# Optimization experiments

Hardware: AMD Instinct MI355X
Metric: run time of the kernel (lower is better)

The kernel has to match this reference:

```python
import jax, jax.numpy as jnp
import numpy as np

B, IN, N, E = 2048, 1024, 64, 128
NEG_SLOPE = 0.01  # torch LeakyReLU default

def setup_inputs() -> dict:
    key = jax.random.key(0)
    k = jax.random.split(key, 5)
    scale_in = 1.0 / np.sqrt(IN)
    scale_ctx = 1.0 / np.sqrt(2 * E)
    return {
        "x": jax.random.normal(k[0], (B, IN), dtype=jnp.float32),
        # stacked per-concept Linear(in_features, 2*emb_size)
        "W_ctx": jax.random.uniform(k[1], (N, IN, 2 * E), jnp.float32, -scale_in, scale_in),
        "b_ctx": jax.random.uniform(k[2], (N, 2 * E), jnp.float32, -scale_in, scale_in),
        # shared Linear(2*emb_size, 1)
        "w_prob": jax.random.uniform(k[3], (2 * E,), jnp.float32, -scale_ctx, scale_ctx),
        "b_prob": jax.random.uniform(k[4], (), jnp.float32, -scale_ctx, scale_ctx),
    }

def reference(x, W_ctx, b_ctx, w_prob, b_prob):
    # context: [B, N, 2E] = LeakyReLU(x @ W_i + b_i) for all concepts i at once
    ctx = jnp.einsum("bi,nio->bno", x, W_ctx) + b_ctx
    ctx = jnp.where(ctx >= 0, ctx, NEG_SLOPE * ctx)
    # shared gate: [B, N]
    c_pred = jax.nn.sigmoid(jnp.einsum("bno,o->bn", ctx, w_prob) + b_prob)
    # gated blend of positive/negative halves -> [B, N, E]
    p = c_pred[..., None]
    c_emb = ctx[..., :E] * p + ctx[..., E:] * (1.0 - p)
    return c_emb, c_pred
```

## Files before the change

kernel.cpp:

```cpp
#include <hip/hip_runtime.h>
#include <hip/hip_bf16.h>

typedef __attribute__((ext_vector_type(4))) short short4v;
typedef __attribute__((ext_vector_type(8))) short short8v;
typedef __attribute__((ext_vector_type(4))) float floatx4;

#define B_ROWS 2048
#define K_DIM  1024
#define N_CON  64
#define TWO_E  256
#define E_DIM  128
#define BM     128
#define BK     64
#define A_STRIDE 72
#define B_STRIDE 72
#define LDSA_BYTES (BM * A_STRIDE * 2)
#define LDSB_BYTES (TWO_E * B_STRIDE * 2)
#define SMEM_BYTES (LDSA_BYTES + LDSB_BYTES)
#define EMB_ELEMS 16777216ULL

static __device__ inline unsigned short bf16bits(float f) {
    __hip_bfloat16 h = __float2bfloat16(f);
    unsigned short u;
    __builtin_memcpy(&u, &h, 2);
    return u;
}

__global__ void __launch_bounds__(256) transpose_w(const float* __restrict__ W,
                                                   unsigned short* __restrict__ Wt) {
    __shared__ unsigned int lds2[64 * 36];
    const int tid = threadIdx.x;
    const int ot = blockIdx.x, ktile = blockIdx.y, n = blockIdx.z;
    const float* src = W + ((size_t)n * K_DIM + (size_t)ktile * 64) * TWO_E + ot * 64;
    unsigned short* dst = Wt + ((size_t)n * TWO_E + (size_t)ot * 64) * K_DIM + ktile * 64;

    const int kp = tid >> 4;
    const int c  = (tid & 15) * 4;
#pragma unroll
    for (int it = 0; it < 2; ++it) {
        const int k0 = it * 32 + kp * 2;
        floatx4 r0 = *(const floatx4*)&src[(size_t)k0 * TWO_E + c];
        floatx4 r1 = *(const floatx4*)&src[(size_t)(k0 + 1) * TWO_E + c];
#pragma unroll
        for (int j = 0; j < 4; ++j) {
            unsigned int d = (unsigned int)bf16bits(r0[j]) |
                             ((unsigned int)bf16bits(r1[j]) << 16);
            lds2[(c + j) * 36 + it * 16 + kp] = d;
        }
    }
    __syncthreads();
#pragma unroll
    for (int it = 0; it < 2; ++it) {
        int q = it * 256 + tid;
        int o = q >> 3, kc = q & 7;
        short8v v = *(short8v*)&lds2[o * 36 + kc * 4];
        *(short8v*)&dst[(size_t)o * K_DIM + kc * 8] = v;
    }
}

template <bool PRET>
__global__ void __launch_bounds__(512, 4)
concept_kernel(const float* __restrict__ x,
               const float* __restrict__ Wc,
               const unsigned short* __restrict__ Wt,
               const float* __restrict__ bc,
               const float* __restrict__ wp,
               const float* __restrict__ bp,
               float* __restrict__ out) {
    __shared__ __align__(16) char smem[SMEM_BYTES];
    unsigned short* ldsA = (unsigned short*)smem;
    unsigned short* ldsB = (unsigned short*)(smem + LDSA_BYTES);

    const int tid  = threadIdx.x;
    const int wave = tid >> 6;
    const int lane = tid & 63;
    const int lg   = lane >> 4;
    const int l15  = lane & 15;
    const int h    = wave >> 2;
    const int og   = wave & 3;
    const int rb = blockIdx.x;
    const int n  = blockIdx.y;

    int otile[4];
#pragma unroll
    for (int oi = 0; oi < 4; ++oi) otile[oi] = og * 32 + (oi & 1) * 16 + (oi & 2) * 64;

    const float* xg = x + (size_t)rb * BM * K_DIM;

    floatx4 acc[4][4];
#pragma unroll
    for (int mi = 0; mi < 4; ++mi)
#pragma unroll
        for (int oi = 0; oi < 4; ++oi) acc[mi][oi] = (floatx4){0.f, 0.f, 0.f, 0.f};

    for (int kt = 0; kt < K_DIM; kt += BK) {
#pragma unroll
        for (int it = 0; it < 4; ++it) {
            int q = it * 512 + tid;
            int r = q >> 4, c = (q & 15) * 4;
            floatx4 v = *(const floatx4*)&xg[(size_t)r * K_DIM + kt + c];
            short4v b;
            b[0] = (short)bf16bits(v[0]);
            b[1] = (short)bf16bits(v[1]);
            b[2] = (short)bf16bits(v[2]);
            b[3] = (short)bf16bits(v[3]);
            *(short4v*)&ldsA[r * A_STRIDE + c] = b;
        }
        if (PRET) {
            const unsigned short* wtg = Wt + (size_t)n * TWO_E * K_DIM;
#pragma unroll
            for (int it = 0; it < 4; ++it) {
                int q = it * 512 + tid;
                int o = q >> 3, ck = q & 7;
                short8v v = *(const short8v*)&wtg[(size_t)o * K_DIM + kt + ck * 8];
                *(short8v*)&ldsB[o * B_STRIDE + ck * 8] = v;
            }
        } else {
            if (tid < 256) {
                const float* wg = Wc + (size_t)n * K_DIM * TWO_E;
#pragma unroll
                for (int it = 0; it < 8; ++it) {
                    short8v v;
#pragma unroll
                    for (int j = 0; j < 8; ++j)
                        v[j] = (short)bf16bits(wg[(size_t)(kt + it * 8 + j) * TWO_E + tid]);
                    *(short8v*)&ldsB[tid * B_STRIDE + it * 8] = v;
                }
            }
        }
        __syncthreads();

#pragma unroll
        for (int ks = 0; ks < 2; ++ks) {
            const int kof = ks * 32 + lg * 8;
            short8v af[4], bfr[4];
#pragma unroll
            for (int mi = 0; mi < 4; ++mi)
                af[mi] = *(short8v*)&ldsA[(h * 64 + mi * 16 + l15) * A_STRIDE + kof];
#pragma unroll
            for (int oi = 0; oi < 4; ++oi)
                bfr[oi] = *(short8v*)&ldsB[(otile[oi] + l15) * B_STRIDE + kof];
#pragma unroll
            for (int mi = 0; mi < 4; ++mi)
#pragma unroll
                for (int oi = 0; oi < 4; ++oi)
                    acc[mi][oi] = __builtin_amdgcn_mfma_f32_16x16x32_bf16(
                        af[mi], bfr[oi], acc[mi][oi], 0, 0, 0);
        }
        __syncthreads();
    }

    float biasf[4], wpf[4];
#pragma unroll
    for (int oi = 0; oi < 4; ++oi) {
        int o = otile[oi] + l15;
        biasf[oi] = bc[n * TWO_E + o];
        wpf[oi]  = wp[o];
    }
#pragma unroll
    for (int mi = 0; mi < 4; ++mi)
#pragma unroll
        for (int oi = 0; oi < 4; ++oi)
#pragma unroll
            for (int j = 0; j < 4; ++j) {
                float v = acc[mi][oi][j] + biasf[oi];
                acc[mi][oi][j] = v >= 0.f ? v : 0.01f * v;
            }

    float* partial = (float*)smem;
    float* pv      = (float*)(smem + 2048);

#pragma unroll
    for (int mi = 0; mi < 4; ++mi)
#pragma unroll
        for (int j = 0; j < 4; ++j) {
            float ps = 0.f;
#pragma unroll
            for (int oi = 0; oi < 4; ++oi) ps += acc[mi][oi][j] * wpf[oi];
            ps += __shfl_xor(ps, 1);
            ps += __shfl_xor(ps, 2);
            ps += __shfl_xor(ps, 4);
            ps += __shfl_xor(ps, 8);
            if (l15 == 0) partial[(h * 64 + mi * 16 + lg * 4 + j) * 4 + og] = ps;
        }
    __syncthreads();

    if (tid < 128) {
        float s = partial[tid * 4] + partial[tid * 4 + 1] + partial[tid * 4 + 2] +
                  partial[tid * 4 + 3] + bp[0];
        float p = 1.f / (1.f + __expf(-s));
        pv[tid] = p;
        size_t bi = (size_t)rb * BM + tid;
        out[EMB_ELEMS + bi * N_CON + n] = p;
    }
    __syncthreads();

#pragma unroll
    for (int mi = 0; mi < 4; ++mi)
#pragma unroll
        for (int oi = 0; oi < 2; ++oi)
#pragma unroll
            for (int j = 0; j < 4; ++j) {
                int row = h * 64 + mi * 16 + lg * 4 + j;
                int e = og * 32 + oi * 16 + l15;
                float p = pv[row];
                float v = acc[mi][oi][j] * p + acc[mi][oi + 2][j] * (1.f - p);
                size_t bi = (size_t)rb * BM + row;
                out[(bi * N_CON + n) * E_DIM + e] = v;
            }
}

extern "C" void kernel_launch(void* const* d_in, const int* in_sizes, int n_in,
                              void* d_out, int out_size, void* d_ws, size_t ws_size,
                              hipStream_t stream) {
    const float* x  = (const float*)d_in[0];
    const float* Wc = (const float*)d_in[1];
    const float* bc = (const float*)d_in[2];
    const float* wp = (const float*)d_in[3];
    const float* bp = (const float*)d_in[4];
    float* out = (float*)d_out;

    const size_t wt_bytes = (size_t)N_CON * K_DIM * TWO_E * 2;
    if (ws_size >= wt_bytes) {
        unsigned short* Wt = (unsigned short*)d_ws;
        transpose_w<<<dim3(4, 16, 64), 256, 0, stream>>>(Wc, Wt);
        concept_kernel<true><<<dim3(16, 64), 512, 0, stream>>>(x, Wc, Wt, bc, wp, bp, out);
    } else {
        concept_kernel<false><<<dim3(16, 64), 512, 0, stream>>>(x, Wc, nullptr, bc, wp, bp, out);
    }
}
```

Measured before the change: 205.3 us.

## Pre-convert x to bf16 and stream tiles into LDS via direct global-to-LDS loads

The prep kernel now also converts x to bf16 in the workspace, alongside the W transpose. The main kernel then loads both A and B tiles with global_load_lds 16-byte direct-to-LDS transfers instead of going through registers. The padded LDS strides are replaced by an XOR swizzle so bank conflicts stay low without padding. This removes the repeated per-block fp32 x reads and conversions and the VGPR staging, at the cost of an extra workspace buffer and a dependence on the swizzle matching the MFMA read pattern.

```diff
diff --git a/kernel.cpp b/kernel.cpp
--- a/kernel.cpp
+++ b/kernel.cpp
@@ -12,12 +12,12 @@
 #define E_DIM  128
 #define BM     128
 #define BK     64
-#define A_STRIDE 72
-#define B_STRIDE 72
-#define LDSA_BYTES (BM * A_STRIDE * 2)
-#define LDSB_BYTES (TWO_E * B_STRIDE * 2)
+#define LDSA_BYTES (BM * BK * 2)
+#define LDSB_BYTES (TWO_E * BK * 2)
 #define SMEM_BYTES (LDSA_BYTES + LDSB_BYTES)
 #define EMB_ELEMS 16777216ULL
+#define WT_BYTES  33554432ULL
+#define XB_BYTES  4194304ULL
 
 static __device__ inline unsigned short bf16bits(float f) {
     __hip_bfloat16 h = __float2bfloat16(f);
@@ -26,8 +26,17 @@
     return u;
 }
 
-__global__ void __launch_bounds__(256) transpose_w(const float* __restrict__ W,
-                                                   unsigned short* __restrict__ Wt) {
+static __device__ inline void dma16(const void* g, void* l) {
+    __builtin_amdgcn_global_load_lds(
+        (const __attribute__((address_space(1))) unsigned int*)g,
+        (__attribute__((address_space(3))) unsigned int*)l,
+        16, 0, 0);
+}
+
+__global__ void __launch_bounds__(256) prep(const float* __restrict__ W,
+                                            const float* __restrict__ x,
+                                            unsigned short* __restrict__ Wt,
+                                            unsigned short* __restrict__ xb) {
     __shared__ unsigned int lds2[64 * 36];
     const int tid = threadIdx.x;
     const int ot = blockIdx.x, ktile = blockIdx.y, n = blockIdx.z;
@@ -56,11 +65,18 @@
         short8v v = *(short8v*)&lds2[o * 36 + kc * 4];
         *(short8v*)&dst[(size_t)o * K_DIM + kc * 8] = v;
     }
+
+    const int bid = blockIdx.x + blockIdx.y * 4 + blockIdx.z * 64;
+    const size_t base = (size_t)bid * 512 + (size_t)tid * 2;
+    unsigned int d = (unsigned int)bf16bits(x[base]) |
+                     ((unsigned int)bf16bits(x[base + 1]) << 16);
+    ((unsigned int*)xb)[base >> 1] = d;
 }
 
 template <bool PRET>
 __global__ void __launch_bounds__(512, 4)
 concept_kernel(const float* __restrict__ x,
+               const unsigned short* __restrict__ xb,
                const float* __restrict__ Wc,
                const unsigned short* __restrict__ Wt,
                const float* __restrict__ bc,
@@ -68,8 +84,8 @@
                const float* __restrict__ bp,
                float* __restrict__ out) {
     __shared__ __align__(16) char smem[SMEM_BYTES];
-    unsigned short* ldsA = (unsigned short*)smem;
-    unsigned short* ldsB = (unsigned short*)(smem + LDSA_BYTES);
+    char* ldsA = smem;
+    char* ldsB = smem + LDSA_BYTES;
 
     const int tid  = threadIdx.x;
     const int wave = tid >> 6;
@@ -85,61 +101,73 @@
 #pragma unroll
     for (int oi = 0; oi < 4; ++oi) otile[oi] = og * 32 + (oi & 1) * 16 + (oi & 2) * 64;
 
+    floatx4 acc[4][4];
+#pragma unroll
+    for (int mi = 0; mi < 4; ++mi)
+#pragma unroll
+        for (int oi = 0; oi < 4; ++oi) acc[mi][oi] = (floatx4){0.f, 0.f, 0.f, 0.f};
+
+    const unsigned short* xrow  = PRET ? xb + (size_t)rb * BM * K_DIM : nullptr;
+    const unsigned short* wbase = PRET ? Wt + (size_t)n * TWO_E * K_DIM : nullptr;
     const float* xg = x + (size_t)rb * BM * K_DIM;
-
-    floatx4 acc[4][4];
-#pragma unroll
-    for (int mi = 0; mi < 4; ++mi)
-#pragma unroll
-        for (int oi = 0; oi < 4; ++oi) acc[mi][oi] = (floatx4){0.f, 0.f, 0.f, 0.f};
+    const float* wg = Wc + (size_t)n * K_DIM * TWO_E;
 
     for (int kt = 0; kt < K_DIM; kt += BK) {
-#pragma unroll
-        for (int it = 0; it < 4; ++it) {
-            int q = it * 512 + tid;
-            int r = q >> 4, c = (q & 15) * 4;
-            floatx4 v = *(const floatx4*)&xg[(size_t)r * K_DIM + kt + c];
-            short4v b;
-            b[0] = (short)bf16bits(v[0]);
-            b[1] = (short)bf16bits(v[1]);
-            b[2] = (short)bf16bits(v[2]);
-            b[3] = (short)bf16bits(v[3]);
-            *(short4v*)&ldsA[r * A_STRIDE + c] = b;
-        }
         if (PRET) {
-            const unsigned short* wtg = Wt + (size_t)n * TWO_E * K_DIM;
+#pragma unroll
+            for (int it = 0; it < 2; ++it) {
+                int c = it * 8 + wave;
+                int s = c * 64 + lane;
+                int r = s >> 3, g = s & 7;
+                dma16(xrow + (size_t)r * K_DIM + kt + ((g ^ (r & 7)) * 8),
+                      ldsA + c * 1024);
+            }
 #pragma unroll
             for (int it = 0; it < 4; ++it) {
-                int q = it * 512 + tid;
-                int o = q >> 3, ck = q & 7;
-                short8v v = *(const short8v*)&wtg[(size_t)o * K_DIM + kt + ck * 8];
-                *(short8v*)&ldsB[o * B_STRIDE + ck * 8] = v;
+                int c = it * 8 + wave;
+                int s = c * 64 + lane;
+                int r = s >> 3, g = s & 7;
+                dma16(wbase + (size_t)r * K_DIM + kt + ((g ^ (r & 7)) * 8),
+                      ldsB + c * 1024);
             }
         } else {
-            if (tid < 256) {
-                const float* wg = Wc + (size_t)n * K_DIM * TWO_E;
-#pragma unroll
-                for (int it = 0; it < 8; ++it) {
-                    short8v v;
-#pragma unroll
-                    for (int j = 0; j < 8; ++j)
-                        v[j] = (short)bf16bits(wg[(size_t)(kt + it * 8 + j) * TWO_E + tid]);
-                    *(short8v*)&ldsB[tid * B_STRIDE + it * 8] = v;
-                }
+#pragma unroll
+            for (int it = 0; it < 2; ++it) {
+                int s = it * 512 + tid;
+                int r = s >> 3, g = s & 7;
+                const float* p = xg + (size_t)r * K_DIM + kt + ((g ^ (r & 7)) * 8);
+                floatx4 v0 = *(const floatx4*)p, v1 = *(const floatx4*)(p + 4);
+                short8v b;
+                b[0] = (short)bf16bits(v0[0]); b[1] = (short)bf16bits(v0[1]);
+                b[2] = (short)bf16bits(v0[2]); b[3] = (short)bf16bits(v0[3]);
+                b[4] = (short)bf16bits(v1[0]); b[5] = (short)bf16bits(v1[1]);
+                b[6] = (short)bf16bits(v1[2]); b[7] = (short)bf16bits(v1[3]);
+                *(short8v*)(ldsA + s * 16) = b;
+            }
+#pragma unroll
+            for (int it = 0; it < 4; ++it) {
+                int s = it * 512 + tid;
+                int r = s >> 3, g = s & 7;
+                int k0 = kt + (g ^ (r & 7)) * 8;
+                short8v b;
+#pragma unroll
+                for (int j = 0; j < 8; ++j)
+                    b[j] = (short)bf16bits(wg[(size_t)(k0 + j) * TWO_E + r]);
+                *(short8v*)(ldsB + s * 16) = b;
             }
         }
         __syncthreads();
 
 #pragma unroll
         for (int ks = 0; ks < 2; ++ks) {
-            const int kof = ks * 32 + lg * 8;
+            const int sw = ((ks * 4 + lg) ^ (l15 & 7)) * 16;
             short8v af[4], bfr[4];
 #pragma unroll
             for (int mi = 0; mi < 4; ++mi)
-                af[mi] = *(short8v*)&ldsA[(h * 64 + mi * 16 + l15) * A_STRIDE + kof];
+                af[mi] = *(const short8v*)(ldsA + (h * 64 + mi * 16 + l15) * 128 + sw);
 #pragma unroll
             for (int oi = 0; oi < 4; ++oi)
-                bfr[oi] = *(short8v*)&ldsB[(otile[oi] + l15) * B_STRIDE + kof];
+                bfr[oi] = *(const short8v*)(ldsB + (otile[oi] + l15) * 128 + sw);
 #pragma unroll
             for (int mi = 0; mi < 4; ++mi)
 #pragma unroll
@@ -220,12 +248,14 @@
     const float* bp = (const float*)d_in[4];
     float* out = (float*)d_out;
 
-    const size_t wt_bytes = (size_t)N_CON * K_DIM * TWO_E * 2;
-    if (ws_size >= wt_bytes) {
+    if (ws_size >= WT_BYTES + XB_BYTES) {
         unsigned short* Wt = (unsigned short*)d_ws;
-        transpose_w<<<dim3(4, 16, 64), 256, 0, stream>>>(Wc, Wt);
-        concept_kernel<true><<<dim3(16, 64), 512, 0, stream>>>(x, Wc, Wt, bc, wp, bp, out);
+        unsigned short* xb = (unsigned short*)((char*)d_ws + WT_BYTES);
+        prep<<<dim3(4, 16, 64), 256, 0, stream>>>(Wc, x, Wt, xb);
+        concept_kernel<true><<<dim3(16, 64), 512, 0, stream>>>(
+            x, xb, Wc, Wt, bc, wp, bp, out);
     } else {
-        concept_kernel<false><<<dim3(16, 64), 512, 0, stream>>>(x, Wc, nullptr, bc, wp, bp, out);
-    }
-}
+        concept_kernel<false><<<dim3(16, 64), 512, 0, stream>>>(
+            x, nullptr, Wc, nullptr, bc, wp, bp, out);
+    }
+}
```

Result: faster. 189.5 us (-7.7%).
